# Performance work log

Hardware: AMD Instinct MI355X
Metric: run time of the kernel (lower is better)

## Reference

```python
import jax, jax.numpy as jnp
import numpy as np

ALPHA = 0.2  # LeakyReLU negative slope


def setup_inputs() -> dict:
    key = jax.random.key(0)
    k1, k2, k3 = jax.random.split(key, 3)
    B, N, F_in, F_out = 8, 2048, 256, 256
    h = jax.random.normal(k1, (B, N, F_in), dtype=jnp.float32)
    adj = jax.random.randint(k2, (B, N, N), 0, 2, dtype=jnp.int32)
    # xavier_uniform for W [F_in, F_out]
    limit = float(np.sqrt(6.0 / (F_in + F_out)))
    W = jax.random.uniform(k3, (F_in, F_out), dtype=jnp.float32, minval=-limit, maxval=limit)
    return {"h": h, "adj": adj, "W": W}


def reference(h, adj, W):
    # h: [B,N,F_in], W: [F_in,F_out] -> Wh: [B,N,F_out]
    Wh = jnp.einsum('bnf,fo->bno', h, W)
    # (Wh_i + Wh_j).sum(-1) == s[p] + s[q] with s = Wh.sum(-1); avoids [B,N,N,F] tensor
    s = Wh.sum(axis=-1)  # [B,N]
    e = jax.nn.leaky_relu(s[:, :, None] + s[:, None, :], negative_slope=ALPHA)  # [B,N,N]
    e = jnp.where(adj == 0, -jnp.inf, e)
    alpha = jax.nn.softmax(e, axis=-1)  # masked softmax over neighbors
    # dropout is identity in eval mode
    h_prime = jnp.einsum('bpq,bqo->bpo', alpha, Wh)  # [B,N,F_out]
    return h_prime
```

## Files before the change

### kernel.cpp

```cpp
#include <hip/hip_runtime.h>
#include <hip/hip_bf16.h>
#include <stdint.h>

#define LEAKY_ALPHA 0.2f

using f32x4 = __attribute__((ext_vector_type(4))) float;
using u32x2 = __attribute__((ext_vector_type(2))) unsigned int;
using u32x4 = __attribute__((ext_vector_type(4))) unsigned int;
using i32x4 = __attribute__((ext_vector_type(4))) int;
using s16x8 = __attribute__((ext_vector_type(8))) short;

static __device__ __forceinline__ unsigned short f2bf(float x) {
  __hip_bfloat16 b = __float2bfloat16(x);
  return __builtin_bit_cast(unsigned short, b);
}

__global__ __launch_bounds__(256) void gat_prep(
    const float* __restrict__ W, __hip_bfloat16* __restrict__ WT,
    float* __restrict__ wsum)
{
  const int o = blockIdx.x;
  const int t = threadIdx.x;
  WT[o * 256 + t] = __float2bfloat16(W[t * 256 + o]);
  float u = W[o * 256 + t];
#pragma unroll
  for (int off = 1; off < 64; off <<= 1) u += __shfl_xor(u, off, 64);
  __shared__ float red[4];
  if ((t & 63) == 0) red[t >> 6] = u;
  __syncthreads();
  if (t == 0) wsum[o] = red[0] + red[1] + red[2] + red[3];
}

__global__ __launch_bounds__(256, 3) void gat_wh2(
    const float* __restrict__ h, const __hip_bfloat16* __restrict__ WT,
    const float* __restrict__ wsum, __hip_bfloat16* __restrict__ WhT,
    float* __restrict__ s)
{
  const int b = blockIdx.x >> 6;
  const int q0 = (blockIdx.x & 63) * 32;
  const int t = threadIdx.x;
  const int wid = t >> 6, lane = t & 63;

  __shared__ __align__(16) unsigned char Bh[32 * 512];
  __shared__ __align__(16) unsigned char Aw[256 * 128];
  __shared__ __align__(16) float wsl[256];

  wsl[t] = wsum[t];
  __syncthreads();

  {
    const int q = t >> 3;
    const int fs = (t & 7) * 32;
    const float* hrow = h + ((size_t)(b * 2048 + q0 + q)) * 256 + fs;
    float sp = 0.f;
#pragma unroll
    for (int c = 0; c < 4; ++c) {
      const f32x4 a  = *(const f32x4*)&hrow[c * 8];
      const f32x4 bq = *(const f32x4*)&hrow[c * 8 + 4];
      const f32x4 wa = *(const f32x4*)&wsl[fs + c * 8];
      const f32x4 wb = *(const f32x4*)&wsl[fs + c * 8 + 4];
      sp += a[0]*wa[0] + a[1]*wa[1] + a[2]*wa[2] + a[3]*wa[3]
          + bq[0]*wb[0] + bq[1]*wb[1] + bq[2]*wb[2] + bq[3]*wb[3];
      u32x4 pk;
      pk[0] = (unsigned)f2bf(a[0])  | ((unsigned)f2bf(a[1])  << 16);
      pk[1] = (unsigned)f2bf(a[2])  | ((unsigned)f2bf(a[3])  << 16);
      pk[2] = (unsigned)f2bf(bq[0]) | ((unsigned)f2bf(bq[1]) << 16);
      pk[3] = (unsigned)f2bf(bq[2]) | ((unsigned)f2bf(bq[3]) << 16);
      const int boff = q * 512 + ((fs * 2 + c * 16) ^ ((q & 7) << 4));
      *(u32x4*)&Bh[boff] = pk;
    }
    sp += __shfl_xor(sp, 1, 64);
    sp += __shfl_xor(sp, 2, 64);
    sp += __shfl_xor(sp, 4, 64);
    if ((t & 7) == 0) s[b * 2048 + q0 + q] = sp;
  }

  f32x4 acc[2][4];
#pragma unroll
  for (int i = 0; i < 2; ++i)
#pragma unroll
    for (int j = 0; j < 4; ++j) acc[i][j] = (f32x4)(0.f);

  for (int it = 0; it < 4; ++it) {
    const int f0 = it * 64;
    __syncthreads();
#pragma unroll
    for (int j = 0; j < 8; ++j) {
      const int o = (t >> 3) + 32 * j;
      const int c = t & 7;
      const u32x4 v = *(const u32x4*)&WT[o * 256 + f0 + c * 8];
      *(u32x4*)&Aw[o * 128 + ((c * 16) ^ ((o & 7) << 4))] = v;
    }
    __syncthreads();
#pragma unroll
    for (int kt = 0; kt < 2; ++kt) {
      const int kb = kt * 64 + ((lane >> 4) << 4);
      s16x8 af[2], bf[4];
#pragma unroll
      for (int qt = 0; qt < 2; ++qt) {
        const int qr = qt * 16 + (lane & 15);
        af[qt] = *(const s16x8*)&Bh[qr * 512 + ((f0 * 2 + kb) ^ ((qr & 7) << 4))];
      }
#pragma unroll
      for (int ot = 0; ot < 4; ++ot) {
        const int orow = wid * 64 + ot * 16 + (lane & 15);
        bf[ot] = *(const s16x8*)&Aw[orow * 128 + (kb ^ ((orow & 7) << 4))];
      }
#pragma unroll
      for (int qt = 0; qt < 2; ++qt)
#pragma unroll
        for (int ot = 0; ot < 4; ++ot)
          acc[qt][ot] = __builtin_amdgcn_mfma_f32_16x16x32_bf16(
              af[qt], bf[ot], acc[qt][ot], 0, 0, 0);
    }
  }

  __hip_bfloat16* __restrict__ WhTb = WhT + (size_t)b * 256 * 2048;
#pragma unroll
  for (int qt = 0; qt < 2; ++qt)
#pragma unroll
    for (int ot = 0; ot < 4; ++ot) {
      const int o = wid * 64 + ot * 16 + (lane & 15);
      const int ql = q0 + qt * 16 + ((lane >> 4) << 2);
      u32x2 pk;
      pk[0] = (unsigned)f2bf(acc[qt][ot][0]) | ((unsigned)f2bf(acc[qt][ot][1]) << 16);
      pk[1] = (unsigned)f2bf(acc[qt][ot][2]) | ((unsigned)f2bf(acc[qt][ot][3]) << 16);
      *(u32x2*)&WhTb[(size_t)o * 2048 + ql] = pk;
    }
}

__global__ __launch_bounds__(512, 4) void gat_attn(
    const int* __restrict__ adj, const float* __restrict__ s,
    const __hip_bfloat16* __restrict__ WhT, float* __restrict__ out)
{
  const int N = 2048;
  const int bid = blockIdx.x;
  const int swz = (bid & 7) * 64 + (bid >> 3);
  const int b = swz >> 6;
  const int p0 = (swz & 63) * 32;
  const int t = threadIdx.x;
  const int wid = t >> 6, lane = t & 63;

  __shared__ __align__(16) unsigned char Bs[2][256 * 128];
  __shared__ __align__(16) unsigned char Wt[2][32 * 128];
  __shared__ __align__(16) float red_sh[8];
  __shared__ __align__(16) float l_sh[32];

  const int ep = t >> 4;
  const int eq4 = (t & 15) * 4;
  const int* __restrict__ adjrow = adj + ((size_t)(b * N + p0 + ep)) * N;
  const float* __restrict__ sB = s + b * N;
  const __hip_bfloat16* __restrict__ WhTb = WhT + (size_t)b * 256 * 2048;

  const int so = t >> 3;
  const int q16 = t & 7;

  i32x4 av = *(const i32x4*)&adjrow[eq4];
  f32x4 sv = *(const f32x4*)&sB[eq4];
  u32x4 breg[4];
#pragma unroll
  for (int j = 0; j < 4; ++j)
    breg[j] = *(const u32x4*)&WhTb[(size_t)(so + 64 * j) * 2048 + q16 * 8];

  const f32x4 s4 = *(const f32x4*)&sB[t * 4];
  float bm = fmaxf(fmaxf(s4[0], s4[1]), fmaxf(s4[2], s4[3]));
#pragma unroll
  for (int off = 1; off < 64; off <<= 1) bm = fmaxf(bm, __shfl_xor(bm, off, 64));
  if (lane == 0) red_sh[wid] = bm;
  const float s_p = sB[p0 + ep];
  __syncthreads();
  float smax = red_sh[0];
#pragma unroll
  for (int k = 1; k < 8; ++k) smax = fmaxf(smax, red_sh[k]);
  const float xm = s_p + smax;
  const float m_p = (xm > 0.f) ? xm : (LEAKY_ALPHA * xm);

  f32x4 acc[2][2];
#pragma unroll
  for (int pt = 0; pt < 2; ++pt)
#pragma unroll
    for (int ot = 0; ot < 2; ++ot) acc[pt][ot] = (f32x4)(0.f);
  float lacc = 0.f;

#define GAT_TILE(BI, QQ)                                                      \
  do {                                                                        \
    float wv[4];                                                              \
    _Pragma("unroll")                                                         \
    for (int i = 0; i < 4; ++i) {                                             \
      const float x = s_p + sv[i];                                            \
      const float le = (x > 0.f) ? x : (LEAKY_ALPHA * x);                     \
      const float w = __expf(le - m_p);                                       \
      wv[i] = (av[i] != 0) ? w : 0.f;                                         \
      lacc += wv[i];                                                          \
    }                                                                         \
    {                                                                         \
      u32x2 pw;                                                               \
      pw[0] = (unsigned)f2bf(wv[0]) | ((unsigned)f2bf(wv[1]) << 16);          \
      pw[1] = (unsigned)f2bf(wv[2]) | ((unsigned)f2bf(wv[3]) << 16);          \
      *(u32x2*)&Wt[BI][ep * 128 + ((eq4 * 2) ^ ((ep & 7) << 4))] = pw;        \
    }                                                                         \
    _Pragma("unroll")                                                         \
    for (int j = 0; j < 4; ++j) {                                             \
      const int o = so + 64 * j;                                              \
      *(u32x4*)&Bs[BI][o * 128 + ((q16 * 16) ^ ((o & 7) << 4))] = breg[j];    \
    }                                                                         \
    if ((QQ) + 64 < N) {                                                      \
      av = *(const i32x4*)&adjrow[(QQ) + 64 + eq4];                           \
      sv = *(const f32x4*)&sB[(QQ) + 64 + eq4];                               \
      _Pragma("unroll")                                                       \
      for (int j = 0; j < 4; ++j)                                             \
        breg[j] = *(const u32x4*)&WhTb[(size_t)(so + 64 * j) * 2048 +         \
                                       (QQ) + 64 + q16 * 8];                  \
    }                                                                         \
    asm volatile("s_waitcnt lgkmcnt(0)" ::: "memory");                        \
    __builtin_amdgcn_s_barrier();                                             \
    asm volatile("" ::: "memory");                                            \
    {                                                                         \
      s16x8 afr[2][2], bfr[2][2];                                             \
      _Pragma("unroll")                                                       \
      for (int pt = 0; pt < 2; ++pt)                                          \
        _Pragma("unroll")                                                     \
        for (int kt = 0; kt < 2; ++kt) {                                      \
          const int pa = pt * 16 + (lane & 15);                               \
          const int kb = kt * 64 + ((lane >> 4) << 4);                        \
          afr[pt][kt] =                                                       \
              *(const s16x8*)&Wt[BI][pa * 128 + (kb ^ ((pa & 7) << 4))];      \
        }                                                                     \
      _Pragma("unroll")                                                       \
      for (int ot = 0; ot < 2; ++ot)                                          \
        _Pragma("unroll")                                                     \
        for (int kt = 0; kt < 2; ++kt) {                                      \
          const int ob = wid * 32 + ot * 16 + (lane & 15);                    \
          const int kb = kt * 64 + ((lane >> 4) << 4);                        \
          bfr[ot][kt] =                                                       \
              *(const s16x8*)&Bs[BI][ob * 128 + (kb ^ ((ob & 7) << 4))];      \
        }                                                                     \
      _Pragma("unroll")                                                       \
      for (int pt = 0; pt < 2; ++pt)                                          \
        _Pragma("unroll")                                                     \
        for (int ot = 0; ot < 2; ++ot)                                        \
          _Pragma("unroll")                                                   \
          for (int kt = 0; kt < 2; ++kt)                                      \
            acc[pt][ot] = __builtin_amdgcn_mfma_f32_16x16x32_bf16(            \
                afr[pt][kt], bfr[ot][kt], acc[pt][ot], 0, 0, 0);              \
    }                                                                         \
  } while (0)

  for (int q0 = 0; q0 < N; q0 += 128) {
    GAT_TILE(0, q0);
    GAT_TILE(1, q0 + 64);
  }
#undef GAT_TILE

  lacc += __shfl_xor(lacc, 1, 64);
  lacc += __shfl_xor(lacc, 2, 64);
  lacc += __shfl_xor(lacc, 4, 64);
  lacc += __shfl_xor(lacc, 8, 64);
  if ((t & 15) == 0) l_sh[ep] = lacc;
  __syncthreads();

#pragma unroll
  for (int pt = 0; pt < 2; ++pt) {
    const f32x4 lv = *(const f32x4*)&l_sh[pt * 16 + ((lane >> 4) << 2)];
    f32x4 inv;
#pragma unroll
    for (int r = 0; r < 4; ++r) inv[r] = 1.f / lv[r];
#pragma unroll
    for (int ot = 0; ot < 2; ++ot) {
      const int o = wid * 32 + ot * 16 + (lane & 15);
#pragma unroll
      for (int r = 0; r < 4; ++r) {
        const int row = p0 + pt * 16 + ((lane >> 4) << 2) + r;
        out[((size_t)(b * N + row)) * 256 + o] = acc[pt][ot][r] * inv[r];
      }
    }
  }
}

extern "C" void kernel_launch(void* const* d_in, const int* in_sizes, int n_in,
                              void* d_out, int out_size, void* d_ws, size_t ws_size,
                              hipStream_t stream) {
  const float* h = (const float*)d_in[0];
  const int* adj = (const int*)d_in[1];
  const float* W = (const float*)d_in[2];
  float* out = (float*)d_out;

  char* ws = (char*)d_ws;
  __hip_bfloat16* WhT = (__hip_bfloat16*)ws;
  float* s = (float*)(ws + (size_t)8 * 1024 * 1024);
  __hip_bfloat16* WT = (__hip_bfloat16*)(ws + (size_t)8 * 1024 * 1024 + 65536);
  float* wsum = (float*)(ws + (size_t)8 * 1024 * 1024 + 65536 + 131072);

  gat_prep<<<256, 256, 0, stream>>>(W, WT, wsum);
  gat_wh2<<<512, 256, 0, stream>>>(h, WT, wsum, WhT, s);
  gat_attn<<<512, 512, 0, stream>>>(adj, s, WhT, out);
}
```

Before: 56.68 us.

## Split attention output features across two blocks to double grid parallelism

The attention kernel now gives each block 128 of the 256 output features for a 32-row tile, using 256 threads and 1024 blocks instead of 512 threads and 512 blocks. Shared memory for the Wh tile halves, and each thread computes 8 attention weights per step instead of 4. The reduction scratch is aliased into the weight buffer, with an extra barrier to keep that safe. The aim is higher occupancy and more blocks in flight. The cost is that the adjacency rows and exponentials are computed twice, once per feature half, which relies on L2 to absorb the duplicate adj reads.

```diff
diff --git a/kernel.cpp b/kernel.cpp
--- a/kernel.cpp
+++ b/kernel.cpp
@@ -129,49 +129,56 @@
     }
 }
 
-__global__ __launch_bounds__(512, 4) void gat_attn(
+__global__ __launch_bounds__(256, 4) void gat_attn(
     const int* __restrict__ adj, const float* __restrict__ s,
     const __hip_bfloat16* __restrict__ WhT, float* __restrict__ out)
 {
   const int N = 2048;
   const int bid = blockIdx.x;
-  const int swz = (bid & 7) * 64 + (bid >> 3);
-  const int b = swz >> 6;
-  const int p0 = (swz & 63) * 32;
+  const int swz = (bid & 7) * 128 + (bid >> 3);
+  const int b = swz >> 7;
+  const int inner = swz & 127;
+  const int p0 = (inner >> 1) * 32;
+  const int o0 = (inner & 1) * 128;
   const int t = threadIdx.x;
   const int wid = t >> 6, lane = t & 63;
 
-  __shared__ __align__(16) unsigned char Bs[2][256 * 128];
+  __shared__ __align__(16) unsigned char Bs[2][128 * 128];
   __shared__ __align__(16) unsigned char Wt[2][32 * 128];
-  __shared__ __align__(16) float red_sh[8];
-  __shared__ __align__(16) float l_sh[32];
-
-  const int ep = t >> 4;
-  const int eq4 = (t & 15) * 4;
+  float* red_sh = (float*)&Wt[0][0];
+  float* l_sh   = (float*)&Wt[0][32];
+
+  const int ep = t >> 3;
+  const int eq8 = (t & 7) * 8;
   const int* __restrict__ adjrow = adj + ((size_t)(b * N + p0 + ep)) * N;
   const float* __restrict__ sB = s + b * N;
-  const __hip_bfloat16* __restrict__ WhTb = WhT + (size_t)b * 256 * 2048;
+  const __hip_bfloat16* __restrict__ WhTb =
+      WhT + (size_t)b * 256 * 2048 + (size_t)o0 * 2048;
 
   const int so = t >> 3;
   const int q16 = t & 7;
 
-  i32x4 av = *(const i32x4*)&adjrow[eq4];
-  f32x4 sv = *(const f32x4*)&sB[eq4];
+  i32x4 av0 = *(const i32x4*)&adjrow[eq8];
+  i32x4 av1 = *(const i32x4*)&adjrow[eq8 + 4];
+  f32x4 sv0 = *(const f32x4*)&sB[eq8];
+  f32x4 sv1 = *(const f32x4*)&sB[eq8 + 4];
   u32x4 breg[4];
 #pragma unroll
   for (int j = 0; j < 4; ++j)
-    breg[j] = *(const u32x4*)&WhTb[(size_t)(so + 64 * j) * 2048 + q16 * 8];
-
-  const f32x4 s4 = *(const f32x4*)&sB[t * 4];
-  float bm = fmaxf(fmaxf(s4[0], s4[1]), fmaxf(s4[2], s4[3]));
+    breg[j] = *(const u32x4*)&WhTb[(size_t)(so + 32 * j) * 2048 + q16 * 8];
+
+  const f32x4 sa = *(const f32x4*)&sB[t * 8];
+  const f32x4 sc = *(const f32x4*)&sB[t * 8 + 4];
+  float bm = fmaxf(fmaxf(fmaxf(sa[0], sa[1]), fmaxf(sa[2], sa[3])),
+                   fmaxf(fmaxf(sc[0], sc[1]), fmaxf(sc[2], sc[3])));
 #pragma unroll
   for (int off = 1; off < 64; off <<= 1) bm = fmaxf(bm, __shfl_xor(bm, off, 64));
   if (lane == 0) red_sh[wid] = bm;
   const float s_p = sB[p0 + ep];
   __syncthreads();
-  float smax = red_sh[0];
-#pragma unroll
-  for (int k = 1; k < 8; ++k) smax = fmaxf(smax, red_sh[k]);
+  const float smax = fmaxf(fmaxf(red_sh[0], red_sh[1]),
+                           fmaxf(red_sh[2], red_sh[3]));
+  __syncthreads();
   const float xm = s_p + smax;
   const float m_p = (xm > 0.f) ? xm : (LEAKY_ALPHA * xm);
 
@@ -184,32 +191,44 @@
 
 #define GAT_TILE(BI, QQ)                                                      \
   do {                                                                        \
-    float wv[4];                                                              \
+    float wv[8];                                                              \
     _Pragma("unroll")                                                         \
     for (int i = 0; i < 4; ++i) {                                             \
-      const float x = s_p + sv[i];                                            \
+      const float x = s_p + sv0[i];                                           \
       const float le = (x > 0.f) ? x : (LEAKY_ALPHA * x);                     \
       const float w = __expf(le - m_p);                                       \
-      wv[i] = (av[i] != 0) ? w : 0.f;                                         \
+      wv[i] = (av0[i] != 0) ? w : 0.f;                                        \
       lacc += wv[i];                                                          \
     }                                                                         \
+    _Pragma("unroll")                                                         \
+    for (int i = 0; i < 4; ++i) {                                             \
+      const float x = s_p + sv1[i];                                           \
+      const float le = (x > 0.f) ? x : (LEAKY_ALPHA * x);                     \
+      const float w = __expf(le - m_p);                                       \
+      wv[4 + i] = (av1[i] != 0) ? w : 0.f;                                    \
+      lacc += wv[4 + i];                                                      \
+    }                                                                         \
     {                                                                         \
-      u32x2 pw;                                                               \
-      pw[0] = (unsigned)f2bf(wv[0]) | ((unsigned)f2bf(wv[1]) << 16);          \
-      pw[1] = (unsigned)f2bf(wv[2]) | ((unsigned)f2bf(wv[3]) << 16);          \
-      *(u32x2*)&Wt[BI][ep * 128 + ((eq4 * 2) ^ ((ep & 7) << 4))] = pw;        \
+      u32x4 pw;                                                               \
+      _Pragma("unroll")                                                       \
+      for (int k2 = 0; k2 < 4; ++k2)                                          \
+        pw[k2] = (unsigned)f2bf(wv[2 * k2]) |                                 \
+                 ((unsigned)f2bf(wv[2 * k2 + 1]) << 16);                      \
+      *(u32x4*)&Wt[BI][ep * 128 + ((eq8 * 2) ^ ((ep & 7) << 4))] = pw;        \
     }                                                                         \
     _Pragma("unroll")                                                         \
     for (int j = 0; j < 4; ++j) {                                             \
-      const int o = so + 64 * j;                                              \
+      const int o = so + 32 * j;                                              \
       *(u32x4*)&Bs[BI][o * 128 + ((q16 * 16) ^ ((o & 7) << 4))] = breg[j];    \
     }                                                                         \
     if ((QQ) + 64 < N) {                                                      \
-      av = *(const i32x4*)&adjrow[(QQ) + 64 + eq4];                           \
-      sv = *(const f32x4*)&sB[(QQ) + 64 + eq4];                               \
+      av0 = *(const i32x4*)&adjrow[(QQ) + 64 + eq8];                          \
+      av1 = *(const i32x4*)&adjrow[(QQ) + 64 + eq8 + 4];                      \
+      sv0 = *(const f32x4*)&sB[(QQ) + 64 + eq8];                              \
+      sv1 = *(const f32x4*)&sB[(QQ) + 64 + eq8 + 4];                          \
       _Pragma("unroll")                                                       \
       for (int j = 0; j < 4; ++j)                                             \
-        breg[j] = *(const u32x4*)&WhTb[(size_t)(so + 64 * j) * 2048 +         \
+        breg[j] = *(const u32x4*)&WhTb[(size_t)(so + 32 * j) * 2048 +         \
                                        (QQ) + 64 + q16 * 8];                  \
     }                                                                         \
     asm volatile("s_waitcnt lgkmcnt(0)" ::: "memory");                        \
@@ -255,8 +274,7 @@
   lacc += __shfl_xor(lacc, 1, 64);
   lacc += __shfl_xor(lacc, 2, 64);
   lacc += __shfl_xor(lacc, 4, 64);
-  lacc += __shfl_xor(lacc, 8, 64);
-  if ((t & 15) == 0) l_sh[ep] = lacc;
+  if ((t & 7) == 0) l_sh[ep] = lacc;
   __syncthreads();
 
 #pragma unroll
@@ -267,7 +285,7 @@
     for (int r = 0; r < 4; ++r) inv[r] = 1.f / lv[r];
 #pragma unroll
     for (int ot = 0; ot < 2; ++ot) {
-      const int o = wid * 32 + ot * 16 + (lane & 15);
+      const int o = o0 + wid * 32 + ot * 16 + (lane & 15);
 #pragma unroll
       for (int r = 0; r < 4; ++r) {
         const int row = p0 + pt * 16 + ((lane >> 4) << 2) + r;
@@ -293,5 +311,5 @@
 
   gat_prep<<<256, 256, 0, stream>>>(W, WT, wsum);
   gat_wh2<<<512, 256, 0, stream>>>(h, WT, wsum, WhT, s);
-  gat_attn<<<512, 512, 0, stream>>>(adj, s, WhT, out);
-}
+  gat_attn<<<1024, 256, 0, stream>>>(adj, s, WhT, out);
+}
```

Result: slower. 64.75 us (+14.2%).
